# Kernel optimization log

Measured on AMD Instinct MI355X. Metric: run time of the kernel, lower is better.

The kernel has to match this reference:

```python
import jax, jax.numpy as jnp
import numpy as np


def a_powers(A, t):
    # A: [K, n, n]; returns [t, K, n, n] = stack(I, A, A^2, ..., A^(t-1))
    K, n, _ = A.shape
    result = jnp.broadcast_to(jnp.eye(n, dtype=A.dtype), (1, K, n, n))
    lift = A
    while result.shape[0] < t:
        result = jnp.concatenate([result, result @ lift], axis=0)
        lift = lift @ lift
    return result[:t]


def fast_conv_real(a, b):
    # a: [len1, K, n, n], b: [batch, len2, K, n] -> conv(b, a): [batch, len1+len2-1, K, n]
    len1 = a.shape[0]
    len2 = b.shape[1]
    T = 2 ** int(np.ceil(np.log2(len1 + len2 - 1)))
    Af = jnp.fft.rfft(a, n=T, axis=0)
    Bf = jnp.fft.rfft(b, n=T, axis=1)
    Cf = jnp.einsum('blki,lkij->blkj', Bf, Af)
    c = jnp.fft.irfft(Cf, n=T, axis=1)
    return c[:, :len1 + len2 - 1]


def setup_inputs() -> dict:
    key = jax.random.key(0)
    k_u, k_x0, k_theta, k_B, k_C = jax.random.split(key, 5)
    batch, length = 8, 4096
    input_size, state_size, output_size = 256, 256, 256
    blk = 2
    K = state_size // blk  # 128
    u = jax.random.normal(k_u, (batch, length, input_size), dtype=jnp.float32)
    x0 = jax.random.normal(k_x0, (batch, K, blk), dtype=jnp.float32)
    # A initialized as K random 2x2 rotation blocks (as in __init__)
    theta = 2 * jnp.pi * jax.random.uniform(k_theta, (K,), dtype=jnp.float32)
    c, s = jnp.cos(theta), jnp.sin(theta)
    A = jnp.stack([jnp.stack([c, s], -1), jnp.stack([-s, c], -1)], -2)  # [K, 2, 2]
    B = jax.random.normal(k_B, (input_size, state_size), dtype=jnp.float32) / (state_size + input_size) ** 0.5
    C = jax.random.normal(k_C, (state_size, output_size), dtype=jnp.float32) / (state_size + output_size) ** 0.5
    return {"u": u, "x0": x0, "A": A, "B": B, "C": C}


def reference(u, x0, A, B, C):
    batch, length, _ = u.shape
    K, blk, _ = A.shape
    Aps = a_powers(A, length + 1)          # [length+1, K, blk, blk]
    uB = (u @ B).reshape(batch, length, K, blk)
    x = fast_conv_real(Aps[:-1], uB)[:, :length]  # [batch, length, K, blk]
    x = x + jnp.einsum('bki,lkij->blkj', x0, Aps[1:])
    new_state = x[:, -1]                    # [batch, K, blk]
    y = x.reshape(batch, length, K * blk) @ C
    return (y, new_state)
```

## Files before the change

### kernel.cpp

```cpp
#include <hip/hip_runtime.h>
#include <hip/hip_bf16.h>
#include <type_traits>

typedef __bf16 bf16x2_t __attribute__((ext_vector_type(2)));
typedef __bf16 bf16x4_t __attribute__((ext_vector_type(4)));
typedef __bf16 bf16x8_t __attribute__((ext_vector_type(8)));
typedef float f32x4 __attribute__((ext_vector_type(4)));

#define BATCH   8
#define LENGTH  4096
#define NSTATE  256
#define KHALF   128
#define MTOT    (BATCH*LENGTH)
#define NCHUNK  128
#define LC      32

__global__ __launch_bounds__(256) void transpose_bc(
    const float* __restrict__ Bsrc, const float* __restrict__ Csrc,
    __bf16* __restrict__ BT, __bf16* __restrict__ CT) {
  const float* src = blockIdx.y ? Csrc : Bsrc;
  __bf16* dst      = blockIdx.y ? CT   : BT;
  int n  = blockIdx.x;
  int kk = threadIdx.x;
  dst[n * 256 + kk] = (__bf16)src[kk * 256 + n];
}

template <typename AT, typename OT>
__global__ __launch_bounds__(256) void gemm_bt(const AT* __restrict__ Ag,
                                               const __bf16* __restrict__ BTg,
                                               OT* __restrict__ Dg) {
  __shared__ __align__(16) __bf16 sA[128][32];
  __shared__ __align__(16) __bf16 sB[128][32];

  const int tid  = threadIdx.x;
  const int lane = tid & 63;
  const int wave = tid >> 6;
  const int wr   = wave >> 1;
  const int wc   = wave & 1;
  const int m_l  = lane & 15;
  const int quad = lane >> 4;
  const int m0   = blockIdx.x * 128;
  const int n0   = blockIdx.y * 128;

  f32x4 acc[4][4];
#pragma unroll
  for (int mi = 0; mi < 4; ++mi)
#pragma unroll
    for (int ni = 0; ni < 4; ++ni)
#pragma unroll
      for (int r = 0; r < 4; ++r) acc[mi][ni][r] = 0.f;

  for (int kc = 0; kc < 256; kc += 32) {
    if constexpr (std::is_same<AT, float>::value) {
#pragma unroll
      for (int i = 0; i < 4; ++i) {
        int s   = tid + i * 256;
        int row = s >> 3;
        int c4  = (s & 7) * 4;
        const float4 v = *(const float4*)(Ag + (size_t)(m0 + row) * 256 + kc + c4);
        bf16x4_t b4;
        b4[0] = (__bf16)v.x; b4[1] = (__bf16)v.y;
        b4[2] = (__bf16)v.z; b4[3] = (__bf16)v.w;
        *(bf16x4_t*)&sA[row][c4] = b4;
      }
    } else {
#pragma unroll
      for (int i = 0; i < 2; ++i) {
        int s   = tid + i * 256;
        int row = s >> 2;
        int c8  = (s & 3) * 8;
        *(int4*)&sA[row][c8] = *(const int4*)(Ag + (size_t)(m0 + row) * 256 + kc + c8);
      }
    }
#pragma unroll
    for (int i = 0; i < 2; ++i) {
      int s   = tid + i * 256;
      int row = s >> 2;
      int c8  = (s & 3) * 8;
      *(int4*)&sB[row][c8] = *(const int4*)(BTg + (size_t)(n0 + row) * 256 + kc + c8);
    }
    __syncthreads();

    bf16x8_t af[4], bfr[4];
#pragma unroll
    for (int mi = 0; mi < 4; ++mi)
      af[mi] = *(const bf16x8_t*)&sA[wr * 64 + mi * 16 + m_l][quad * 8];
#pragma unroll
    for (int ni = 0; ni < 4; ++ni)
      bfr[ni] = *(const bf16x8_t*)&sB[wc * 64 + ni * 16 + m_l][quad * 8];
#pragma unroll
    for (int mi = 0; mi < 4; ++mi)
#pragma unroll
      for (int ni = 0; ni < 4; ++ni)
        acc[mi][ni] = __builtin_amdgcn_mfma_f32_16x16x32_bf16(af[mi], bfr[ni], acc[mi][ni], 0, 0, 0);
    __syncthreads();
  }

#pragma unroll
  for (int mi = 0; mi < 4; ++mi)
#pragma unroll
    for (int ni = 0; ni < 4; ++ni)
#pragma unroll
      for (int r = 0; r < 4; ++r) {
        int row = m0 + wr * 64 + mi * 16 + quad * 4 + r;
        int col = n0 + wc * 64 + ni * 16 + m_l;
        if constexpr (std::is_same<OT, float>::value)
          Dg[(size_t)row * 256 + col] = acc[mi][ni][r];
        else
          Dg[(size_t)row * 256 + col] = (__bf16)acc[mi][ni][r];
      }
}

__global__ __launch_bounds__(128) void scan_partial(const __bf16* __restrict__ uB,
                                                    const float* __restrict__ Aarr,
                                                    float2* __restrict__ P) {
  const int k     = threadIdx.x;
  const int chunk = blockIdx.x;
  const int b     = blockIdx.y;
  const float c = Aarr[4 * k], s = Aarr[4 * k + 1];
  float hr = 0.f, hi = 0.f;
  const __bf16* p = uB + ((size_t)(b * LENGTH + chunk * LC)) * 256 + 2 * k;
#pragma unroll 8
  for (int j = 0; j < LC; ++j) {
    bf16x2_t u2 = *(const bf16x2_t*)p;
    p += 256;
    float t = fmaf(hr, c, fmaf(-hi, s, (float)u2[0]));
    hi      = fmaf(hr, s, fmaf( hi, c, (float)u2[1]));
    hr = t;
  }
  P[((size_t)b * NCHUNK + chunk) * KHALF + k] = make_float2(hr, hi);
}

__global__ __launch_bounds__(128) void scan_carry(const float* __restrict__ Aarr,
                                                  const float* __restrict__ x0,
                                                  const float2* __restrict__ P,
                                                  float2* __restrict__ H,
                                                  float* __restrict__ state_out) {
  const int k = threadIdx.x;
  const int b = blockIdx.x;
  const float c = Aarr[4 * k], s = Aarr[4 * k + 1];
  float wr = c, wi = s;
#pragma unroll
  for (int i = 0; i < 5; ++i) {
    float nr = wr * wr - wi * wi;
    float ni = 2.f * wr * wi;
    wr = nr; wi = ni;
  }
  float hr = x0[b * 256 + 2 * k], hi = x0[b * 256 + 2 * k + 1];
#pragma unroll 4
  for (int ch = 0; ch < NCHUNK; ++ch) {
    H[((size_t)b * NCHUNK + ch) * KHALF + k] = make_float2(hr, hi);
    float2 pv = P[((size_t)b * NCHUNK + ch) * KHALF + k];
    float t = fmaf(hr, wr, fmaf(-hi, wi, pv.x));
    hi      = fmaf(hr, wi, fmaf( hi, wr, pv.y));
    hr = t;
  }
  state_out[b * 256 + 2 * k]     = hr;
  state_out[b * 256 + 2 * k + 1] = hi;
}

__global__ __launch_bounds__(128) void scan_apply(const __bf16* __restrict__ uB,
                                                  const float* __restrict__ Aarr,
                                                  const float2* __restrict__ H,
                                                  __bf16* __restrict__ X) {
  const int k     = threadIdx.x;
  const int chunk = blockIdx.x;
  const int b     = blockIdx.y;
  const float c = Aarr[4 * k], s = Aarr[4 * k + 1];
  float2 h = H[((size_t)b * NCHUNK + chunk) * KHALF + k];
  float hr = h.x, hi = h.y;
  const __bf16* pin = uB + ((size_t)(b * LENGTH + chunk * LC)) * 256 + 2 * k;
  __bf16*       po  = (__bf16*)X + ((size_t)(b * LENGTH + chunk * LC)) * 256 + 2 * k;
#pragma unroll 8
  for (int j = 0; j < LC; ++j) {
    bf16x2_t u2 = *(const bf16x2_t*)pin;
    pin += 256;
    float t = fmaf(hr, c, fmaf(-hi, s, (float)u2[0]));
    hi      = fmaf(hr, s, fmaf( hi, c, (float)u2[1]));
    hr = t;
    bf16x2_t o;
    o[0] = (__bf16)hr; o[1] = (__bf16)hi;
    *(bf16x2_t*)po = o;
    po += 256;
  }
}

extern "C" void kernel_launch(void* const* d_in, const int* in_sizes, int n_in,
                              void* d_out, int out_size, void* d_ws, size_t ws_size,
                              hipStream_t stream) {
  const float* u  = (const float*)d_in[0];
  const float* x0 = (const float*)d_in[1];
  const float* A  = (const float*)d_in[2];
  const float* B  = (const float*)d_in[3];
  const float* C  = (const float*)d_in[4];

  float* y         = (float*)d_out;
  float* state_out = y + (size_t)MTOT * 256;

  char* ws = (char*)d_ws;
  __bf16* BT = (__bf16*)ws;  ws += 256 * 256 * 2;
  __bf16* CT = (__bf16*)ws;  ws += 256 * 256 * 2;
  __bf16* uB = (__bf16*)ws;  ws += (size_t)MTOT * 256 * 2;
  __bf16* X  = (__bf16*)ws;  ws += (size_t)MTOT * 256 * 2;
  float2* P  = (float2*)ws;  ws += (size_t)BATCH * NCHUNK * KHALF * sizeof(float2);
  float2* H  = (float2*)ws;  ws += (size_t)BATCH * NCHUNK * KHALF * sizeof(float2);

  transpose_bc<<<dim3(256, 2), 256, 0, stream>>>(B, C, BT, CT);
  gemm_bt<float, __bf16><<<dim3(MTOT / 128, 2), 256, 0, stream>>>(u, BT, uB);
  scan_partial<<<dim3(NCHUNK, BATCH), 128, 0, stream>>>(uB, A, P);
  scan_carry<<<dim3(BATCH), 128, 0, stream>>>(A, x0, P, H, state_out);
  scan_apply<<<dim3(NCHUNK, BATCH), 128, 0, stream>>>(uB, A, H, X);
  gemm_bt<__bf16, float><<<dim3(MTOT / 128, 2), 256, 0, stream>>>(X, CT, y);
}
```

Before: 136.1 us.

## Fuse chunk scans into GEMM kernels and parallelize carry scan across lanes

The chunk-local partial scan is moved into the epilogue of the first GEMM, working on the tile held in shared memory. The apply scan is moved into the prologue of the second GEMM, so the X intermediate is no longer written to or read from global memory. The serial carry scan over 128 chunks becomes a wave-level parallel prefix scan using shuffles and precomputed rotation powers. Each GEMM now stages a full 128x256 K-panel in shared memory with an XOR swizzle and reads B fragments directly from global. The 64KB of LDS per block can lower occupancy, and in the second GEMM the scan is computed redundantly by both N-tile blocks.

```diff
diff --git a/kernel.cpp b/kernel.cpp
--- a/kernel.cpp
+++ b/kernel.cpp
@@ -1,19 +1,18 @@
 #include <hip/hip_runtime.h>
 #include <hip/hip_bf16.h>
-#include <type_traits>
 
 typedef __bf16 bf16x2_t __attribute__((ext_vector_type(2)));
-typedef __bf16 bf16x4_t __attribute__((ext_vector_type(4)));
 typedef __bf16 bf16x8_t __attribute__((ext_vector_type(8)));
 typedef float f32x4 __attribute__((ext_vector_type(4)));
 
 #define BATCH   8
 #define LENGTH  4096
-#define NSTATE  256
 #define KHALF   128
 #define MTOT    (BATCH*LENGTH)
 #define NCHUNK  128
 #define LC      32
+
+#define SWZ(ch, row) ((ch) ^ ((row) & 7))
 
 __global__ __launch_bounds__(256) void transpose_bc(
     const float* __restrict__ Bsrc, const float* __restrict__ Csrc,
@@ -25,22 +24,34 @@
   dst[n * 256 + kk] = (__bf16)src[kk * 256 + n];
 }
 
-template <typename AT, typename OT>
-__global__ __launch_bounds__(256) void gemm_bt(const AT* __restrict__ Ag,
-                                               const __bf16* __restrict__ BTg,
-                                               OT* __restrict__ Dg) {
-  __shared__ __align__(16) __bf16 sA[128][32];
-  __shared__ __align__(16) __bf16 sB[128][32];
+__global__ __launch_bounds__(256) void gemm1_fused(
+    const float* __restrict__ u, const __bf16* __restrict__ BT,
+    const float* __restrict__ Aarr,
+    __bf16* __restrict__ uB, float2* __restrict__ P) {
+  __shared__ __align__(16) __bf16 sA[128 * 256];
 
   const int tid  = threadIdx.x;
   const int lane = tid & 63;
   const int wave = tid >> 6;
-  const int wr   = wave >> 1;
-  const int wc   = wave & 1;
-  const int m_l  = lane & 15;
-  const int quad = lane >> 4;
+  const int wr   = wave >> 1, wc = wave & 1;
+  const int m_l  = lane & 15, quad = lane >> 4;
   const int m0   = blockIdx.x * 128;
   const int n0   = blockIdx.y * 128;
+  const int b    = m0 >> 12;
+  const int t0   = m0 & 4095;
+
+#pragma unroll
+  for (int i = 0; i < 16; ++i) {
+    int s   = tid + i * 256;
+    int row = s >> 5, ch = s & 31;
+    const float4* g = (const float4*)(u + (size_t)(m0 + row) * 256 + ch * 8);
+    float4 a = g[0], c = g[1];
+    bf16x8_t v;
+    v[0]=(__bf16)a.x; v[1]=(__bf16)a.y; v[2]=(__bf16)a.z; v[3]=(__bf16)a.w;
+    v[4]=(__bf16)c.x; v[5]=(__bf16)c.y; v[6]=(__bf16)c.z; v[7]=(__bf16)c.w;
+    *(bf16x8_t*)&sA[row * 256 + SWZ(ch, row) * 8] = v;
+  }
+  __syncthreads();
 
   f32x4 acc[4][4];
 #pragma unroll
@@ -50,50 +61,192 @@
 #pragma unroll
       for (int r = 0; r < 4; ++r) acc[mi][ni][r] = 0.f;
 
-  for (int kc = 0; kc < 256; kc += 32) {
-    if constexpr (std::is_same<AT, float>::value) {
-#pragma unroll
-      for (int i = 0; i < 4; ++i) {
-        int s   = tid + i * 256;
-        int row = s >> 3;
-        int c4  = (s & 7) * 4;
-        const float4 v = *(const float4*)(Ag + (size_t)(m0 + row) * 256 + kc + c4);
-        bf16x4_t b4;
-        b4[0] = (__bf16)v.x; b4[1] = (__bf16)v.y;
-        b4[2] = (__bf16)v.z; b4[3] = (__bf16)v.w;
-        *(bf16x4_t*)&sA[row][c4] = b4;
-      }
-    } else {
-#pragma unroll
-      for (int i = 0; i < 2; ++i) {
-        int s   = tid + i * 256;
-        int row = s >> 2;
-        int c8  = (s & 3) * 8;
-        *(int4*)&sA[row][c8] = *(const int4*)(Ag + (size_t)(m0 + row) * 256 + kc + c8);
-      }
-    }
-#pragma unroll
-    for (int i = 0; i < 2; ++i) {
-      int s   = tid + i * 256;
-      int row = s >> 2;
-      int c8  = (s & 3) * 8;
-      *(int4*)&sB[row][c8] = *(const int4*)(BTg + (size_t)(n0 + row) * 256 + kc + c8);
-    }
-    __syncthreads();
-
+#pragma unroll
+  for (int kc8 = 0; kc8 < 8; ++kc8) {
     bf16x8_t af[4], bfr[4];
 #pragma unroll
-    for (int mi = 0; mi < 4; ++mi)
-      af[mi] = *(const bf16x8_t*)&sA[wr * 64 + mi * 16 + m_l][quad * 8];
-#pragma unroll
-    for (int ni = 0; ni < 4; ++ni)
-      bfr[ni] = *(const bf16x8_t*)&sB[wc * 64 + ni * 16 + m_l][quad * 8];
+    for (int mi = 0; mi < 4; ++mi) {
+      int row = wr * 64 + mi * 16 + m_l;
+      int c   = kc8 * 4 + quad;
+      af[mi] = *(const bf16x8_t*)&sA[row * 256 + SWZ(c, row) * 8];
+    }
+#pragma unroll
+    for (int ni = 0; ni < 4; ++ni) {
+      int n = n0 + wc * 64 + ni * 16 + m_l;
+      bfr[ni] = *(const bf16x8_t*)(BT + (size_t)n * 256 + kc8 * 32 + quad * 8);
+    }
 #pragma unroll
     for (int mi = 0; mi < 4; ++mi)
 #pragma unroll
       for (int ni = 0; ni < 4; ++ni)
         acc[mi][ni] = __builtin_amdgcn_mfma_f32_16x16x32_bf16(af[mi], bfr[ni], acc[mi][ni], 0, 0, 0);
-    __syncthreads();
+  }
+  __syncthreads();
+
+  __bf16* sT = sA;
+#pragma unroll
+  for (int mi = 0; mi < 4; ++mi)
+#pragma unroll
+    for (int ni = 0; ni < 4; ++ni)
+#pragma unroll
+      for (int r = 0; r < 4; ++r) {
+        int row = wr * 64 + mi * 16 + quad * 4 + r;
+        int col = wc * 64 + ni * 16 + m_l;
+        __bf16 val = (__bf16)acc[mi][ni][r];
+        uB[(size_t)(m0 + row) * 256 + n0 + col] = val;
+        sT[row * 128 + SWZ(col >> 3, row) * 8 + (col & 7)] = val;
+      }
+  __syncthreads();
+
+  {
+    int kl  = tid & 63;
+    int chl = tid >> 6;
+    int kg  = (n0 >> 1) + kl;
+    float cc = Aarr[4 * kg], sv = Aarr[4 * kg + 1];
+    float hr = 0.f, hi = 0.f;
+#pragma unroll 8
+    for (int j = 0; j < LC; ++j) {
+      int row = chl * 32 + j;
+      int col = 2 * kl;
+      bf16x2_t v2 = *(const bf16x2_t*)&sT[row * 128 + SWZ(col >> 3, row) * 8 + (col & 7)];
+      float t = fmaf(hr, cc, fmaf(-hi, sv, (float)v2[0]));
+      hi      = fmaf(hr, sv, fmaf( hi, cc, (float)v2[1]));
+      hr = t;
+    }
+    int chg = (t0 >> 5) + chl;
+    P[((size_t)b * NCHUNK + chg) * KHALF + kg] = make_float2(hr, hi);
+  }
+}
+
+__global__ __launch_bounds__(256) void scan_carry2(
+    const float* __restrict__ Aarr, const float* __restrict__ x0,
+    const float2* __restrict__ P, float2* __restrict__ H,
+    float* __restrict__ state_out) {
+  const int lane = threadIdx.x & 63;
+  const int wv   = threadIdx.x >> 6;
+  const int p    = blockIdx.x * 4 + wv;
+  const int b    = p >> 7, k = p & 127;
+  const float cc = Aarr[4 * k], sv = Aarr[4 * k + 1];
+
+  float wr = cc, wi = sv;
+#pragma unroll
+  for (int i = 0; i < 5; ++i) { float nr = wr*wr - wi*wi; wi = 2.f*wr*wi; wr = nr; }
+  float Wr[6], Wi[6];
+  Wr[0] = wr*wr - wi*wi; Wi[0] = 2.f*wr*wi;
+#pragma unroll
+  for (int s = 1; s < 6; ++s) { Wr[s] = Wr[s-1]*Wr[s-1] - Wi[s-1]*Wi[s-1]; Wi[s] = 2.f*Wr[s-1]*Wi[s-1]; }
+
+  float2 P0 = P[((size_t)b * NCHUNK + 2 * lane)     * KHALF + k];
+  float2 P1 = P[((size_t)b * NCHUNK + 2 * lane + 1) * KHALF + k];
+  float qr = fmaf(wr, P0.x, fmaf(-wi, P0.y, P1.x));
+  float qi = fmaf(wr, P0.y, fmaf( wi, P0.x, P1.y));
+  float Sr = qr, Si = qi;
+#pragma unroll
+  for (int s = 0; s < 6; ++s) {
+    float tr = __shfl_up(Sr, 1 << s, 64);
+    float ti = __shfl_up(Si, 1 << s, 64);
+    if (lane >= (1 << s)) {
+      float nSr = fmaf(Wr[s], tr, fmaf(-Wi[s], ti, Sr));
+      float nSi = fmaf(Wr[s], ti, fmaf( Wi[s], tr, Si));
+      Sr = nSr; Si = nSi;
+    }
+  }
+  float Ar = __shfl_up(Sr, 1, 64), Ai = __shfl_up(Si, 1, 64);
+  if (lane == 0) { Ar = 0.f; Ai = 0.f; }
+  float pr = 1.f, pi = 0.f;
+#pragma unroll
+  for (int s = 0; s < 6; ++s)
+    if ((lane >> s) & 1) { float nr = pr*Wr[s] - pi*Wi[s]; pi = pr*Wi[s] + pi*Wr[s]; pr = nr; }
+
+  float x0r = x0[b * 256 + 2 * k], x0i = x0[b * 256 + 2 * k + 1];
+  float H0r = fmaf(pr, x0r, fmaf(-pi, x0i, Ar));
+  float H0i = fmaf(pr, x0i, fmaf( pi, x0r, Ai));
+  H[((size_t)b * NCHUNK + 2 * lane) * KHALF + k] = make_float2(H0r, H0i);
+  float H1r = fmaf(wr, H0r, fmaf(-wi, H0i, P0.x));
+  float H1i = fmaf(wr, H0i, fmaf( wi, H0r, P0.y));
+  H[((size_t)b * NCHUNK + 2 * lane + 1) * KHALF + k] = make_float2(H1r, H1i);
+  if (lane == 63) {
+    state_out[b * 256 + 2 * k]     = fmaf(wr, H1r, fmaf(-wi, H1i, P1.x));
+    state_out[b * 256 + 2 * k + 1] = fmaf(wr, H1i, fmaf( wi, H1r, P1.y));
+  }
+}
+
+__global__ __launch_bounds__(256) void gemm2_fused(
+    const __bf16* __restrict__ uB, const float* __restrict__ Aarr,
+    const float2* __restrict__ H, const __bf16* __restrict__ CT,
+    float* __restrict__ Y) {
+  __shared__ __align__(16) __bf16 sX[128 * 256];
+
+  const int tid  = threadIdx.x;
+  const int lane = tid & 63;
+  const int wave = tid >> 6;
+  const int wr   = wave >> 1, wc = wave & 1;
+  const int m_l  = lane & 15, quad = lane >> 4;
+  const int m0   = blockIdx.x * 128;
+  const int n0   = blockIdx.y * 128;
+  const int b    = m0 >> 12;
+  const int t0   = m0 & 4095;
+
+#pragma unroll
+  for (int i = 0; i < 16; ++i) {
+    int s   = tid + i * 256;
+    int row = s >> 5, ch = s & 31;
+    *(bf16x8_t*)&sX[row * 256 + SWZ(ch, row) * 8] =
+        *(const bf16x8_t*)(uB + (size_t)(m0 + row) * 256 + ch * 8);
+  }
+  __syncthreads();
+
+  {
+    int k   = tid & 127;
+    int ch0 = tid >> 7;
+    float cc = Aarr[4 * k], sv = Aarr[4 * k + 1];
+#pragma unroll
+    for (int pass = 0; pass < 2; ++pass) {
+      int chl = ch0 + 2 * pass;
+      float2 h = H[((size_t)b * NCHUNK + (t0 >> 5) + chl) * KHALF + k];
+      float hr = h.x, hi = h.y;
+#pragma unroll 8
+      for (int j = 0; j < LC; ++j) {
+        int row = chl * 32 + j;
+        int idx = row * 256 + SWZ(k >> 2, row) * 8 + ((2 * k) & 7);
+        bf16x2_t v2 = *(const bf16x2_t*)&sX[idx];
+        float t = fmaf(hr, cc, fmaf(-hi, sv, (float)v2[0]));
+        hi      = fmaf(hr, sv, fmaf( hi, cc, (float)v2[1]));
+        hr = t;
+        bf16x2_t o; o[0] = (__bf16)hr; o[1] = (__bf16)hi;
+        *(bf16x2_t*)&sX[idx] = o;
+      }
+    }
+  }
+  __syncthreads();
+
+  f32x4 acc[4][4];
+#pragma unroll
+  for (int mi = 0; mi < 4; ++mi)
+#pragma unroll
+    for (int ni = 0; ni < 4; ++ni)
+#pragma unroll
+      for (int r = 0; r < 4; ++r) acc[mi][ni][r] = 0.f;
+
+#pragma unroll
+  for (int kc8 = 0; kc8 < 8; ++kc8) {
+    bf16x8_t af[4], bfr[4];
+#pragma unroll
+    for (int mi = 0; mi < 4; ++mi) {
+      int row = wr * 64 + mi * 16 + m_l;
+      int c   = kc8 * 4 + quad;
+      af[mi] = *(const bf16x8_t*)&sX[row * 256 + SWZ(c, row) * 8];
+    }
+#pragma unroll
+    for (int ni = 0; ni < 4; ++ni) {
+      int n = n0 + wc * 64 + ni * 16 + m_l;
+      bfr[ni] = *(const bf16x8_t*)(CT + (size_t)n * 256 + kc8 * 32 + quad * 8);
+    }
+#pragma unroll
+    for (int mi = 0; mi < 4; ++mi)
+#pragma unroll
+      for (int ni = 0; ni < 4; ++ni)
+        acc[mi][ni] = __builtin_amdgcn_mfma_f32_16x16x32_bf16(af[mi], bfr[ni], acc[mi][ni], 0, 0, 0);
   }
 
 #pragma unroll
@@ -104,85 +257,8 @@
       for (int r = 0; r < 4; ++r) {
         int row = m0 + wr * 64 + mi * 16 + quad * 4 + r;
         int col = n0 + wc * 64 + ni * 16 + m_l;
-        if constexpr (std::is_same<OT, float>::value)
-          Dg[(size_t)row * 256 + col] = acc[mi][ni][r];
-        else
-          Dg[(size_t)row * 256 + col] = (__bf16)acc[mi][ni][r];
+        Y[(size_t)row * 256 + col] = acc[mi][ni][r];
       }
-}
-
-__global__ __launch_bounds__(128) void scan_partial(const __bf16* __restrict__ uB,
-                                                    const float* __restrict__ Aarr,
-                                                    float2* __restrict__ P) {
-  const int k     = threadIdx.x;
-  const int chunk = blockIdx.x;
-  const int b     = blockIdx.y;
-  const float c = Aarr[4 * k], s = Aarr[4 * k + 1];
-  float hr = 0.f, hi = 0.f;
-  const __bf16* p = uB + ((size_t)(b * LENGTH + chunk * LC)) * 256 + 2 * k;
-#pragma unroll 8
-  for (int j = 0; j < LC; ++j) {
-    bf16x2_t u2 = *(const bf16x2_t*)p;
-    p += 256;
-    float t = fmaf(hr, c, fmaf(-hi, s, (float)u2[0]));
-    hi      = fmaf(hr, s, fmaf( hi, c, (float)u2[1]));
-    hr = t;
-  }
-  P[((size_t)b * NCHUNK + chunk) * KHALF + k] = make_float2(hr, hi);
-}
-
-__global__ __launch_bounds__(128) void scan_carry(const float* __restrict__ Aarr,
-                                                  const float* __restrict__ x0,
-                                                  const float2* __restrict__ P,
-                                                  float2* __restrict__ H,
-                                                  float* __restrict__ state_out) {
-  const int k = threadIdx.x;
-  const int b = blockIdx.x;
-  const float c = Aarr[4 * k], s = Aarr[4 * k + 1];
-  float wr = c, wi = s;
-#pragma unroll
-  for (int i = 0; i < 5; ++i) {
-    float nr = wr * wr - wi * wi;
-    float ni = 2.f * wr * wi;
-    wr = nr; wi = ni;
-  }
-  float hr = x0[b * 256 + 2 * k], hi = x0[b * 256 + 2 * k + 1];
-#pragma unroll 4
-  for (int ch = 0; ch < NCHUNK; ++ch) {
-    H[((size_t)b * NCHUNK + ch) * KHALF + k] = make_float2(hr, hi);
-    float2 pv = P[((size_t)b * NCHUNK + ch) * KHALF + k];
-    float t = fmaf(hr, wr, fmaf(-hi, wi, pv.x));
-    hi      = fmaf(hr, wi, fmaf( hi, wr, pv.y));
-    hr = t;
-  }
-  state_out[b * 256 + 2 * k]     = hr;
-  state_out[b * 256 + 2 * k + 1] = hi;
-}
-
-__global__ __launch_bounds__(128) void scan_apply(const __bf16* __restrict__ uB,
-                                                  const float* __restrict__ Aarr,
-                                                  const float2* __restrict__ H,
-                                                  __bf16* __restrict__ X) {
-  const int k     = threadIdx.x;
-  const int chunk = blockIdx.x;
-  const int b     = blockIdx.y;
-  const float c = Aarr[4 * k], s = Aarr[4 * k + 1];
-  float2 h = H[((size_t)b * NCHUNK + chunk) * KHALF + k];
-  float hr = h.x, hi = h.y;
-  const __bf16* pin = uB + ((size_t)(b * LENGTH + chunk * LC)) * 256 + 2 * k;
-  __bf16*       po  = (__bf16*)X + ((size_t)(b * LENGTH + chunk * LC)) * 256 + 2 * k;
-#pragma unroll 8
-  for (int j = 0; j < LC; ++j) {
-    bf16x2_t u2 = *(const bf16x2_t*)pin;
-    pin += 256;
-    float t = fmaf(hr, c, fmaf(-hi, s, (float)u2[0]));
-    hi      = fmaf(hr, s, fmaf( hi, c, (float)u2[1]));
-    hr = t;
-    bf16x2_t o;
-    o[0] = (__bf16)hr; o[1] = (__bf16)hi;
-    *(bf16x2_t*)po = o;
-    po += 256;
-  }
 }
 
 extern "C" void kernel_launch(void* const* d_in, const int* in_sizes, int n_in,
@@ -201,14 +277,11 @@
   __bf16* BT = (__bf16*)ws;  ws += 256 * 256 * 2;
   __bf16* CT = (__bf16*)ws;  ws += 256 * 256 * 2;
   __bf16* uB = (__bf16*)ws;  ws += (size_t)MTOT * 256 * 2;
-  __bf16* X  = (__bf16*)ws;  ws += (size_t)MTOT * 256 * 2;
   float2* P  = (float2*)ws;  ws += (size_t)BATCH * NCHUNK * KHALF * sizeof(float2);
   float2* H  = (float2*)ws;  ws += (size_t)BATCH * NCHUNK * KHALF * sizeof(float2);
 
   transpose_bc<<<dim3(256, 2), 256, 0, stream>>>(B, C, BT, CT);
-  gemm_bt<float, __bf16><<<dim3(MTOT / 128, 2), 256, 0, stream>>>(u, BT, uB);
-  scan_partial<<<dim3(NCHUNK, BATCH), 128, 0, stream>>>(uB, A, P);
-  scan_carry<<<dim3(BATCH), 128, 0, stream>>>(A, x0, P, H, state_out);
-  scan_apply<<<dim3(NCHUNK, BATCH), 128, 0, stream>>>(uB, A, H, X);
-  gemm_bt<__bf16, float><<<dim3(MTOT / 128, 2), 256, 0, stream>>>(X, CT, y);
-}
+  gemm1_fused<<<dim3(MTOT / 128, 2), 256, 0, stream>>>(u, BT, A, uB, P);
+  scan_carry2<<<dim3(256), 256, 0, stream>>>(A, x0, P, H, state_out);
+  gemm2_fused<<<dim3(MTOT / 128, 2), 256, 0, stream>>>(uB, A, H, CT, y);
+}
```

Measured after the change: 121.8 us. -10.5%, faster.
